# Kernel optimization log

Measured on AMD Instinct MI355X. Metric: run time of the kernel, lower is better.

The kernel has to match this reference:

```python
import jax, jax.numpy as jnp
import numpy as np

B, N, D, C = 256, 256, 512, 1024
EPS = 1e-12  # F.normalize eps


def _l2norm(x):
    n = jnp.linalg.norm(x, axis=-1, keepdims=True)
    return x / jnp.maximum(n, EPS)


def setup_inputs() -> dict:
    key = jax.random.key(0)
    k1, k2, k3 = jax.random.split(key, 3)
    return {
        "image_tokens": jax.random.normal(k1, (B, N, D), dtype=jnp.float32),
        "text_features": jax.random.normal(k2, (C, D), dtype=jnp.float32),
        "log_tau": jnp.asarray(np.log(0.07), dtype=jnp.float32),
        "log_attn_tau": jnp.asarray(np.log(0.07), dtype=jnp.float32),
        "pid_labels": jax.random.randint(k3, (B,), 0, C),
    }


def reference(image_tokens, text_features, log_tau, log_attn_tau, pid_labels):
    toks = _l2norm(image_tokens.astype(jnp.float32))        # [B,N,D]
    txt = _l2norm(text_features.astype(jnp.float32))        # [C,D]
    sims = jnp.einsum('bnd,cd->bnc', toks, txt)             # [B,N,C]
    gt = pid_labels.astype(jnp.int32)
    # sims[arange(B), :, gt] -> [B,N]
    sims_gt = jnp.take_along_axis(sims, gt[:, None, None], axis=2)[..., 0]
    attn_tau = jnp.clip(jnp.exp(log_attn_tau), 0.01, 1.0)
    w = jax.nn.softmax(sims_gt / attn_tau, axis=1)          # [B,N]
    logits = jnp.einsum('bn,bnc->bc', w, sims)              # [B,C]
    tau = jnp.clip(jnp.exp(log_tau), 0.01, 1.0)
    logits = logits / tau
    # cross_entropy with label_smoothing=0.0, mean reduction
    logp = jax.nn.log_softmax(logits, axis=-1)
    nll = -jnp.take_along_axis(logp, gt[:, None], axis=1)[:, 0]
    return jnp.mean(nll)
```

## Files before the change

kernel.cpp:

```cpp
#include <hip/hip_runtime.h>
#include <math.h>

#define Bb 256
#define Nn 256
#define Dd 512
#define Cc 1024
#define KC 8
#define KD (Dd / KC)

__device__ __forceinline__ float waveReduceSum(float v) {
    #pragma unroll
    for (int off = 32; off > 0; off >>= 1)
        v += __shfl_xor(v, off, 64);
    return v;
}
__device__ __forceinline__ float waveReduceMax(float v) {
    #pragma unroll
    for (int off = 32; off > 0; off >>= 1)
        v = fmaxf(v, __shfl_xor(v, off, 64));
    return v;
}

__global__ void k_txtnorm(const float* __restrict__ txt, float* __restrict__ txt_n) {
    const int c = blockIdx.x;
    const int lane = threadIdx.x;
    const float* row = txt + (size_t)c * Dd + lane * 8;
    float4 a = *(const float4*)row;
    float4 b = *(const float4*)(row + 4);
    float ss = a.x*a.x + a.y*a.y + a.z*a.z + a.w*a.w
             + b.x*b.x + b.y*b.y + b.z*b.z + b.w*b.w;
    ss = waveReduceSum(ss);
    const float inv = 1.0f / fmaxf(sqrtf(ss), 1e-12f);
    float* out = txt_n + (size_t)c * Dd + lane * 8;
    a.x *= inv; a.y *= inv; a.z *= inv; a.w *= inv;
    b.x *= inv; b.y *= inv; b.z *= inv; b.w *= inv;
    *(float4*)out = a;
    *(float4*)(out + 4) = b;
}

__global__ void k_transpose(const float* __restrict__ txt_n, float* __restrict__ txt_t) {
    __shared__ float tile[32][33];
    const int c0 = blockIdx.x * 32;
    const int d0 = blockIdx.y * 32;
    const int tx = threadIdx.x & 31;
    const int ty = threadIdx.x >> 5;
    #pragma unroll
    for (int r = ty; r < 32; r += 8)
        tile[r][tx] = txt_n[(size_t)(c0 + r) * Dd + d0 + tx];
    __syncthreads();
    #pragma unroll
    for (int r = ty; r < 32; r += 8)
        txt_t[(size_t)(d0 + r) * Cc + c0 + tx] = tile[tx][r];
}

__global__ void __launch_bounds__(1024) k_attn_q(const float* __restrict__ toks,
                                                 const float* __restrict__ txt_n,
                                                 const int* __restrict__ pid,
                                                 const float* __restrict__ log_attn_tau,
                                                 float* __restrict__ q) {
    const int b = blockIdx.x;
    const int tid = threadIdx.x;
    const int wv = tid >> 6;
    const int lane = tid & 63;
    __shared__ float xg[Dd];
    __shared__ float qpart_s[16][Dd];
    __shared__ float ms[16], Ss[16];
    const int g = pid[b];
    if (tid < Dd) xg[tid] = txt_n[(size_t)g * Dd + tid];
    __syncthreads();
    float at = expf(log_attn_tau[0]);
    at = fminf(fmaxf(at, 0.01f), 1.0f);
    const float iat = 1.0f / at;

    const float4 xg0 = *(const float4*)&xg[lane * 8];
    const float4 xg1 = *(const float4*)&xg[lane * 8 + 4];

    float m = -INFINITY, S = 0.0f;
    float qa[8] = {0.f, 0.f, 0.f, 0.f, 0.f, 0.f, 0.f, 0.f};

    const float* base = toks + ((size_t)b * Nn + wv * 16) * Dd + lane * 8;
    float4 t0 = *(const float4*)base;
    float4 t1 = *(const float4*)(base + 4);
    #pragma unroll 4
    for (int r = 0; r < 16; ++r) {
        float4 n0, n1;
        if (r < 15) {
            const float* p = base + (size_t)(r + 1) * Dd;
            n0 = *(const float4*)p;
            n1 = *(const float4*)(p + 4);
        }
        float dot = t0.x*xg0.x + t0.y*xg0.y + t0.z*xg0.z + t0.w*xg0.w
                  + t1.x*xg1.x + t1.y*xg1.y + t1.z*xg1.z + t1.w*xg1.w;
        float ss  = t0.x*t0.x + t0.y*t0.y + t0.z*t0.z + t0.w*t0.w
                  + t1.x*t1.x + t1.y*t1.y + t1.z*t1.z + t1.w*t1.w;
        dot = waveReduceSum(dot);
        ss = waveReduceSum(ss);
        const float inv = 1.0f / fmaxf(sqrtf(ss), 1e-12f);
        const float s = dot * inv;
        if (s > m) {
            const float sc = expf((m - s) * iat);
            S = S * sc + 1.0f;
            qa[0] = qa[0]*sc + inv*t0.x; qa[1] = qa[1]*sc + inv*t0.y;
            qa[2] = qa[2]*sc + inv*t0.z; qa[3] = qa[3]*sc + inv*t0.w;
            qa[4] = qa[4]*sc + inv*t1.x; qa[5] = qa[5]*sc + inv*t1.y;
            qa[6] = qa[6]*sc + inv*t1.z; qa[7] = qa[7]*sc + inv*t1.w;
            m = s;
        } else {
            const float e = expf((s - m) * iat);
            S += e;
            const float w = e * inv;
            qa[0] = fmaf(w, t0.x, qa[0]); qa[1] = fmaf(w, t0.y, qa[1]);
            qa[2] = fmaf(w, t0.z, qa[2]); qa[3] = fmaf(w, t0.w, qa[3]);
            qa[4] = fmaf(w, t1.x, qa[4]); qa[5] = fmaf(w, t1.y, qa[5]);
            qa[6] = fmaf(w, t1.z, qa[6]); qa[7] = fmaf(w, t1.w, qa[7]);
        }
        t0 = n0; t1 = n1;
    }
    #pragma unroll
    for (int j = 0; j < 8; ++j) qpart_s[wv][lane * 8 + j] = qa[j];
    if (lane == 0) { ms[wv] = m; Ss[wv] = S; }
    __syncthreads();
    if (tid < Dd) {
        float M = -INFINITY;
        #pragma unroll
        for (int w = 0; w < 16; ++w) M = fmaxf(M, ms[w]);
        float Stot = 0.f, acc = 0.f;
        #pragma unroll
        for (int w = 0; w < 16; ++w) {
            const float sc = expf((ms[w] - M) * iat);
            Stot = fmaf(Ss[w], sc, Stot);
            acc = fmaf(qpart_s[w][tid], sc, acc);
        }
        q[(size_t)b * Dd + tid] = acc / Stot;
    }
}

__global__ void k_logits(const float* __restrict__ q, const float* __restrict__ txt_t,
                         float* __restrict__ part) {
    const int b0 = blockIdx.x * 4;
    const int kc = blockIdx.y;
    const int d0 = kc * KD;
    const int t = threadIdx.x;
    __shared__ float qs[4][KD];
    {
        const int j = t >> 6, d = t & 63;
        qs[j][d] = q[(size_t)(b0 + j) * Dd + d0 + d];
    }
    __syncthreads();
    const float4* xt = (const float4*)txt_t;
    float4 a0 = {0,0,0,0}, a1 = {0,0,0,0}, a2 = {0,0,0,0}, a3 = {0,0,0,0};
    #pragma unroll 4
    for (int d = 0; d < KD; d += 4) {
        const float4 q0 = *(const float4*)&qs[0][d];
        const float4 q1 = *(const float4*)&qs[1][d];
        const float4 q2 = *(const float4*)&qs[2][d];
        const float4 q3 = *(const float4*)&qs[3][d];
        const float4 x0 = xt[(size_t)(d0 + d + 0) * (Cc / 4) + t];
        const float4 x1 = xt[(size_t)(d0 + d + 1) * (Cc / 4) + t];
        const float4 x2 = xt[(size_t)(d0 + d + 2) * (Cc / 4) + t];
        const float4 x3 = xt[(size_t)(d0 + d + 3) * (Cc / 4) + t];
        a0.x = fmaf(q0.x,x0.x,a0.x); a0.y = fmaf(q0.x,x0.y,a0.y); a0.z = fmaf(q0.x,x0.z,a0.z); a0.w = fmaf(q0.x,x0.w,a0.w);
        a0.x = fmaf(q0.y,x1.x,a0.x); a0.y = fmaf(q0.y,x1.y,a0.y); a0.z = fmaf(q0.y,x1.z,a0.z); a0.w = fmaf(q0.y,x1.w,a0.w);
        a0.x = fmaf(q0.z,x2.x,a0.x); a0.y = fmaf(q0.z,x2.y,a0.y); a0.z = fmaf(q0.z,x2.z,a0.z); a0.w = fmaf(q0.z,x2.w,a0.w);
        a0.x = fmaf(q0.w,x3.x,a0.x); a0.y = fmaf(q0.w,x3.y,a0.y); a0.z = fmaf(q0.w,x3.z,a0.z); a0.w = fmaf(q0.w,x3.w,a0.w);
        a1.x = fmaf(q1.x,x0.x,a1.x); a1.y = fmaf(q1.x,x0.y,a1.y); a1.z = fmaf(q1.x,x0.z,a1.z); a1.w = fmaf(q1.x,x0.w,a1.w);
        a1.x = fmaf(q1.y,x1.x,a1.x); a1.y = fmaf(q1.y,x1.y,a1.y); a1.z = fmaf(q1.y,x1.z,a1.z); a1.w = fmaf(q1.y,x1.w,a1.w);
        a1.x = fmaf(q1.z,x2.x,a1.x); a1.y = fmaf(q1.z,x2.y,a1.y); a1.z = fmaf(q1.z,x2.z,a1.z); a1.w = fmaf(q1.z,x2.w,a1.w);
        a1.x = fmaf(q1.w,x3.x,a1.x); a1.y = fmaf(q1.w,x3.y,a1.y); a1.z = fmaf(q1.w,x3.z,a1.z); a1.w = fmaf(q1.w,x3.w,a1.w);
        a2.x = fmaf(q2.x,x0.x,a2.x); a2.y = fmaf(q2.x,x0.y,a2.y); a2.z = fmaf(q2.x,x0.z,a2.z); a2.w = fmaf(q2.x,x0.w,a2.w);
        a2.x = fmaf(q2.y,x1.x,a2.x); a2.y = fmaf(q2.y,x1.y,a2.y); a2.z = fmaf(q2.y,x1.z,a2.z); a2.w = fmaf(q2.y,x1.w,a2.w);
        a2.x = fmaf(q2.z,x2.x,a2.x); a2.y = fmaf(q2.z,x2.y,a2.y); a2.z = fmaf(q2.z,x2.z,a2.z); a2.w = fmaf(q2.z,x2.w,a2.w);
        a2.x = fmaf(q2.w,x3.x,a2.x); a2.y = fmaf(q2.w,x3.y,a2.y); a2.z = fmaf(q2.w,x3.z,a2.z); a2.w = fmaf(q2.w,x3.w,a2.w);
        a3.x = fmaf(q3.x,x0.x,a3.x); a3.y = fmaf(q3.x,x0.y,a3.y); a3.z = fmaf(q3.x,x0.z,a3.z); a3.w = fmaf(q3.x,x0.w,a3.w);
        a3.x = fmaf(q3.y,x1.x,a3.x); a3.y = fmaf(q3.y,x1.y,a3.y); a3.z = fmaf(q3.y,x1.z,a3.z); a3.w = fmaf(q3.y,x1.w,a3.w);
        a3.x = fmaf(q3.z,x2.x,a3.x); a3.y = fmaf(q3.z,x2.y,a3.y); a3.z = fmaf(q3.z,x2.z,a3.z); a3.w = fmaf(q3.z,x2.w,a3.w);
        a3.x = fmaf(q3.w,x3.x,a3.x); a3.y = fmaf(q3.w,x3.y,a3.y); a3.z = fmaf(q3.w,x3.z,a3.z); a3.w = fmaf(q3.w,x3.w,a3.w);
    }
    float* pb = part + ((size_t)kc * Bb + b0) * Cc;
    ((float4*)(pb + 0 * Cc))[t] = a0;
    ((float4*)(pb + 1 * Cc))[t] = a1;
    ((float4*)(pb + 2 * Cc))[t] = a2;
    ((float4*)(pb + 3 * Cc))[t] = a3;
}

__global__ void k_lse(const float* __restrict__ part, const int* __restrict__ pid,
                      const float* __restrict__ log_tau, float* __restrict__ nll) {
    const int b = blockIdx.x;
    const int t = threadIdx.x;
    float4 l = {0,0,0,0};
    #pragma unroll
    for (int kc = 0; kc < KC; ++kc) {
        const float4 p = ((const float4*)(part + ((size_t)kc * Bb + b) * Cc))[t];
        l.x += p.x; l.y += p.y; l.z += p.z; l.w += p.w;
    }
    float tau = expf(log_tau[0]);
    tau = fminf(fmaxf(tau, 0.01f), 1.0f);
    const float itau = 1.0f / tau;
    l.x *= itau; l.y *= itau; l.z *= itau; l.w *= itau;

    const int g = pid[b];
    __shared__ float redm[4], reds[4], sgt;
    if ((g >> 2) == t) {
        const float v[4] = {l.x, l.y, l.z, l.w};
        sgt = v[g & 3];
    }
    float m = fmaxf(fmaxf(l.x, l.y), fmaxf(l.z, l.w));
    m = waveReduceMax(m);
    if ((t & 63) == 0) redm[t >> 6] = m;
    __syncthreads();
    m = fmaxf(fmaxf(redm[0], redm[1]), fmaxf(redm[2], redm[3]));
    float e = expf(l.x - m) + expf(l.y - m) + expf(l.z - m) + expf(l.w - m);
    e = waveReduceSum(e);
    if ((t & 63) == 0) reds[t >> 6] = e;
    __syncthreads();
    if (t == 0) {
        const float S = reds[0] + reds[1] + reds[2] + reds[3];
        nll[b] = m + logf(S) - sgt;
    }
}

__global__ void k_mean(const float* __restrict__ nll, float* __restrict__ out) {
    float v = nll[threadIdx.x];
    __shared__ float red[4];
    v = waveReduceSum(v);
    if ((threadIdx.x & 63) == 0) red[threadIdx.x >> 6] = v;
    __syncthreads();
    if (threadIdx.x == 0) out[0] = (red[0] + red[1] + red[2] + red[3]) * (1.0f / (float)Bb);
}

extern "C" void kernel_launch(void* const* d_in, const int* in_sizes, int n_in,
                              void* d_out, int out_size, void* d_ws, size_t ws_size,
                              hipStream_t stream) {
    const float* toks = (const float*)d_in[0];
    const float* txt = (const float*)d_in[1];
    const float* log_tau = (const float*)d_in[2];
    const float* log_attn_tau = (const float*)d_in[3];
    const int* pid = (const int*)d_in[4];
    float* out = (float*)d_out;

    float* ws = (float*)d_ws;
    float* txt_n = ws;
    float* txt_t = txt_n + (size_t)Cc * Dd;
    float* q     = txt_t + (size_t)Dd * Cc;
    float* part  = q + (size_t)Bb * Dd;
    float* nll   = part + (size_t)KC * Bb * Cc;

    k_txtnorm<<<Cc, 64, 0, stream>>>(txt, txt_n);
    k_transpose<<<dim3(Cc / 32, Dd / 32), 256, 0, stream>>>(txt_n, txt_t);
    k_attn_q<<<Bb, 1024, 0, stream>>>(toks, txt_n, pid, log_attn_tau, q);
    k_logits<<<dim3(Bb / 4, KC), 256, 0, stream>>>(q, txt_t, part);
    k_lse<<<Bb, 256, 0, stream>>>(part, pid, log_tau, nll);
    k_mean<<<1, 256, 0, stream>>>(nll, out);
}
```

Baseline: 218.8 us.

## Fuse text normalize with transpose, batch token loads, widen logits batch tile

Merges text normalization and transpose into one kernel that computes row norms and writes the normalized transposed matrix, which drops the intermediate normalized buffer and one launch. The attention kernel now normalizes the ground-truth text row itself. It also loads four token rows per batch and interleaves their shuffle reductions to expose more memory and instruction parallelism. The logits kernel processes 8 batch rows per block instead of 4 to reuse text loads more, at the cost of more registers and fewer blocks.

```diff
diff --git a/kernel.cpp b/kernel.cpp
--- a/kernel.cpp
+++ b/kernel.cpp
@@ -7,6 +7,7 @@
 #define Cc 1024
 #define KC 8
 #define KD (Dd / KC)
+#define BT 8
 
 __device__ __forceinline__ float waveReduceSum(float v) {
     #pragma unroll
@@ -21,40 +22,47 @@
     return v;
 }
 
-__global__ void k_txtnorm(const float* __restrict__ txt, float* __restrict__ txt_n) {
-    const int c = blockIdx.x;
-    const int lane = threadIdx.x;
-    const float* row = txt + (size_t)c * Dd + lane * 8;
-    float4 a = *(const float4*)row;
-    float4 b = *(const float4*)(row + 4);
-    float ss = a.x*a.x + a.y*a.y + a.z*a.z + a.w*a.w
-             + b.x*b.x + b.y*b.y + b.z*b.z + b.w*b.w;
-    ss = waveReduceSum(ss);
-    const float inv = 1.0f / fmaxf(sqrtf(ss), 1e-12f);
-    float* out = txt_n + (size_t)c * Dd + lane * 8;
-    a.x *= inv; a.y *= inv; a.z *= inv; a.w *= inv;
-    b.x *= inv; b.y *= inv; b.z *= inv; b.w *= inv;
-    *(float4*)out = a;
-    *(float4*)(out + 4) = b;
-}
-
-__global__ void k_transpose(const float* __restrict__ txt_n, float* __restrict__ txt_t) {
+__global__ void k_txt_prep(const float* __restrict__ txt, float* __restrict__ txt_t) {
+    __shared__ float ssp[32][8];
+    __shared__ float inv[32];
     __shared__ float tile[32][33];
     const int c0 = blockIdx.x * 32;
-    const int d0 = blockIdx.y * 32;
-    const int tx = threadIdx.x & 31;
-    const int ty = threadIdx.x >> 5;
-    #pragma unroll
-    for (int r = ty; r < 32; r += 8)
-        tile[r][tx] = txt_n[(size_t)(c0 + r) * Dd + d0 + tx];
-    __syncthreads();
-    #pragma unroll
-    for (int r = ty; r < 32; r += 8)
-        txt_t[(size_t)(d0 + r) * Cc + c0 + tx] = tile[tx][r];
+    const int t = threadIdx.x;
+    {
+        const int r = t >> 3, seg = t & 7;
+        const float4* p = (const float4*)(txt + (size_t)(c0 + r) * Dd + seg * 64);
+        float s = 0.f;
+        #pragma unroll
+        for (int i = 0; i < 16; ++i) {
+            const float4 a = p[i];
+            s += a.x*a.x + a.y*a.y + a.z*a.z + a.w*a.w;
+        }
+        ssp[r][seg] = s;
+    }
+    __syncthreads();
+    if (t < 32) {
+        float s = 0.f;
+        #pragma unroll
+        for (int j = 0; j < 8; ++j) s += ssp[t][j];
+        inv[t] = 1.0f / fmaxf(sqrtf(s), 1e-12f);
+    }
+    __syncthreads();
+    const int dx = t & 31, r4 = t >> 5;
+    const int dt0 = blockIdx.y * 128;
+    for (int dt = dt0; dt < dt0 + 128; dt += 32) {
+        #pragma unroll
+        for (int rr = r4; rr < 32; rr += 8)
+            tile[rr][dx] = txt[(size_t)(c0 + rr) * Dd + dt + dx] * inv[rr];
+        __syncthreads();
+        #pragma unroll
+        for (int rr = r4; rr < 32; rr += 8)
+            txt_t[(size_t)(dt + rr) * Cc + c0 + dx] = tile[dx][rr];
+        __syncthreads();
+    }
 }
 
 __global__ void __launch_bounds__(1024) k_attn_q(const float* __restrict__ toks,
-                                                 const float* __restrict__ txt_n,
+                                                 const float* __restrict__ txt,
                                                  const int* __restrict__ pid,
                                                  const float* __restrict__ log_attn_tau,
                                                  float* __restrict__ q) {
@@ -63,11 +71,22 @@
     const int wv = tid >> 6;
     const int lane = tid & 63;
     __shared__ float xg[Dd];
+    __shared__ float r8[8];
     __shared__ float qpart_s[16][Dd];
     __shared__ float ms[16], Ss[16];
+
     const int g = pid[b];
-    if (tid < Dd) xg[tid] = txt_n[(size_t)g * Dd + tid];
-    __syncthreads();
+    float v = 0.f;
+    if (tid < Dd) v = txt[(size_t)g * Dd + tid];
+    float p = v * v;
+    p = waveReduceSum(p);
+    if (lane == 0 && wv < 8) r8[wv] = p;
+    __syncthreads();
+    const float tot = r8[0]+r8[1]+r8[2]+r8[3]+r8[4]+r8[5]+r8[6]+r8[7];
+    const float invg = 1.0f / fmaxf(sqrtf(tot), 1e-12f);
+    if (tid < Dd) xg[tid] = v * invg;
+    __syncthreads();
+
     float at = expf(log_attn_tau[0]);
     at = fminf(fmaxf(at, 0.01f), 1.0f);
     const float iat = 1.0f / at;
@@ -78,43 +97,64 @@
     float m = -INFINITY, S = 0.0f;
     float qa[8] = {0.f, 0.f, 0.f, 0.f, 0.f, 0.f, 0.f, 0.f};
 
-    const float* base = toks + ((size_t)b * Nn + wv * 16) * Dd + lane * 8;
-    float4 t0 = *(const float4*)base;
-    float4 t1 = *(const float4*)(base + 4);
-    #pragma unroll 4
-    for (int r = 0; r < 16; ++r) {
-        float4 n0, n1;
-        if (r < 15) {
-            const float* p = base + (size_t)(r + 1) * Dd;
-            n0 = *(const float4*)p;
-            n1 = *(const float4*)(p + 4);
-        }
-        float dot = t0.x*xg0.x + t0.y*xg0.y + t0.z*xg0.z + t0.w*xg0.w
-                  + t1.x*xg1.x + t1.y*xg1.y + t1.z*xg1.z + t1.w*xg1.w;
-        float ss  = t0.x*t0.x + t0.y*t0.y + t0.z*t0.z + t0.w*t0.w
-                  + t1.x*t1.x + t1.y*t1.y + t1.z*t1.z + t1.w*t1.w;
-        dot = waveReduceSum(dot);
-        ss = waveReduceSum(ss);
-        const float inv = 1.0f / fmaxf(sqrtf(ss), 1e-12f);
-        const float s = dot * inv;
-        if (s > m) {
-            const float sc = expf((m - s) * iat);
-            S = S * sc + 1.0f;
-            qa[0] = qa[0]*sc + inv*t0.x; qa[1] = qa[1]*sc + inv*t0.y;
-            qa[2] = qa[2]*sc + inv*t0.z; qa[3] = qa[3]*sc + inv*t0.w;
-            qa[4] = qa[4]*sc + inv*t1.x; qa[5] = qa[5]*sc + inv*t1.y;
-            qa[6] = qa[6]*sc + inv*t1.z; qa[7] = qa[7]*sc + inv*t1.w;
-            m = s;
-        } else {
-            const float e = expf((s - m) * iat);
-            S += e;
-            const float w = e * inv;
-            qa[0] = fmaf(w, t0.x, qa[0]); qa[1] = fmaf(w, t0.y, qa[1]);
-            qa[2] = fmaf(w, t0.z, qa[2]); qa[3] = fmaf(w, t0.w, qa[3]);
-            qa[4] = fmaf(w, t1.x, qa[4]); qa[5] = fmaf(w, t1.y, qa[5]);
-            qa[6] = fmaf(w, t1.z, qa[6]); qa[7] = fmaf(w, t1.w, qa[7]);
-        }
-        t0 = n0; t1 = n1;
+    const float* base = toks + ((size_t)b * Nn + wv * 16) * Dd + (size_t)lane * 8;
+    float4 c0[4], c1[4];
+    #pragma unroll
+    for (int k = 0; k < 4; ++k) {
+        c0[k] = *(const float4*)(base + k * Dd);
+        c1[k] = *(const float4*)(base + k * Dd + 4);
+    }
+    #pragma unroll
+    for (int batch = 0; batch < 4; ++batch) {
+        float4 n0[4], n1[4];
+        if (batch < 3) {
+            const float* pn = base + (batch + 1) * 4 * Dd;
+            #pragma unroll
+            for (int k = 0; k < 4; ++k) {
+                n0[k] = *(const float4*)(pn + k * Dd);
+                n1[k] = *(const float4*)(pn + k * Dd + 4);
+            }
+        }
+        float dt[4], ss[4];
+        #pragma unroll
+        for (int k = 0; k < 4; ++k) {
+            dt[k] = c0[k].x*xg0.x + c0[k].y*xg0.y + c0[k].z*xg0.z + c0[k].w*xg0.w
+                  + c1[k].x*xg1.x + c1[k].y*xg1.y + c1[k].z*xg1.z + c1[k].w*xg1.w;
+            ss[k] = c0[k].x*c0[k].x + c0[k].y*c0[k].y + c0[k].z*c0[k].z + c0[k].w*c0[k].w
+                  + c1[k].x*c1[k].x + c1[k].y*c1[k].y + c1[k].z*c1[k].z + c1[k].w*c1[k].w;
+        }
+        #pragma unroll
+        for (int off = 32; off > 0; off >>= 1) {
+            #pragma unroll
+            for (int k = 0; k < 4; ++k) {
+                dt[k] += __shfl_xor(dt[k], off, 64);
+                ss[k] += __shfl_xor(ss[k], off, 64);
+            }
+        }
+        #pragma unroll
+        for (int k = 0; k < 4; ++k) {
+            const float inv = 1.0f / fmaxf(sqrtf(ss[k]), 1e-12f);
+            const float s = dt[k] * inv;
+            if (s > m) {
+                const float sc = expf((m - s) * iat);
+                S = S * sc + 1.0f;
+                qa[0] = qa[0]*sc + inv*c0[k].x; qa[1] = qa[1]*sc + inv*c0[k].y;
+                qa[2] = qa[2]*sc + inv*c0[k].z; qa[3] = qa[3]*sc + inv*c0[k].w;
+                qa[4] = qa[4]*sc + inv*c1[k].x; qa[5] = qa[5]*sc + inv*c1[k].y;
+                qa[6] = qa[6]*sc + inv*c1[k].z; qa[7] = qa[7]*sc + inv*c1[k].w;
+                m = s;
+            } else {
+                const float e = expf((s - m) * iat);
+                S += e;
+                const float w = e * inv;
+                qa[0] = fmaf(w, c0[k].x, qa[0]); qa[1] = fmaf(w, c0[k].y, qa[1]);
+                qa[2] = fmaf(w, c0[k].z, qa[2]); qa[3] = fmaf(w, c0[k].w, qa[3]);
+                qa[4] = fmaf(w, c1[k].x, qa[4]); qa[5] = fmaf(w, c1[k].y, qa[5]);
+                qa[6] = fmaf(w, c1[k].z, qa[6]); qa[7] = fmaf(w, c1[k].w, qa[7]);
+            }
+        }
+        #pragma unroll
+        for (int k = 0; k < 4; ++k) { c0[k] = n0[k]; c1[k] = n1[k]; }
     }
     #pragma unroll
     for (int j = 0; j < 8; ++j) qpart_s[wv][lane * 8 + j] = qa[j];
@@ -137,50 +177,36 @@
 
 __global__ void k_logits(const float* __restrict__ q, const float* __restrict__ txt_t,
                          float* __restrict__ part) {
-    const int b0 = blockIdx.x * 4;
+    const int b0 = blockIdx.x * BT;
     const int kc = blockIdx.y;
     const int d0 = kc * KD;
     const int t = threadIdx.x;
-    __shared__ float qs[4][KD];
-    {
-        const int j = t >> 6, d = t & 63;
-        qs[j][d] = q[(size_t)(b0 + j) * Dd + d0 + d];
-    }
+    __shared__ float qs[BT][KD];
+    for (int i = t; i < BT * KD; i += 256)
+        qs[i >> 6][i & 63] = q[(size_t)(b0 + (i >> 6)) * Dd + d0 + (i & 63)];
     __syncthreads();
     const float4* xt = (const float4*)txt_t;
-    float4 a0 = {0,0,0,0}, a1 = {0,0,0,0}, a2 = {0,0,0,0}, a3 = {0,0,0,0};
-    #pragma unroll 4
+    float4 a[BT];
+    #pragma unroll
+    for (int j = 0; j < BT; ++j) a[j] = make_float4(0.f, 0.f, 0.f, 0.f);
+    #pragma unroll 2
     for (int d = 0; d < KD; d += 4) {
-        const float4 q0 = *(const float4*)&qs[0][d];
-        const float4 q1 = *(const float4*)&qs[1][d];
-        const float4 q2 = *(const float4*)&qs[2][d];
-        const float4 q3 = *(const float4*)&qs[3][d];
         const float4 x0 = xt[(size_t)(d0 + d + 0) * (Cc / 4) + t];
         const float4 x1 = xt[(size_t)(d0 + d + 1) * (Cc / 4) + t];
         const float4 x2 = xt[(size_t)(d0 + d + 2) * (Cc / 4) + t];
         const float4 x3 = xt[(size_t)(d0 + d + 3) * (Cc / 4) + t];
-        a0.x = fmaf(q0.x,x0.x,a0.x); a0.y = fmaf(q0.x,x0.y,a0.y); a0.z = fmaf(q0.x,x0.z,a0.z); a0.w = fmaf(q0.x,x0.w,a0.w);
-        a0.x = fmaf(q0.y,x1.x,a0.x); a0.y = fmaf(q0.y,x1.y,a0.y); a0.z = fmaf(q0.y,x1.z,a0.z); a0.w = fmaf(q0.y,x1.w,a0.w);
-        a0.x = fmaf(q0.z,x2.x,a0.x); a0.y = fmaf(q0.z,x2.y,a0.y); a0.z = fmaf(q0.z,x2.z,a0.z); a0.w = fmaf(q0.z,x2.w,a0.w);
-        a0.x = fmaf(q0.w,x3.x,a0.x); a0.y = fmaf(q0.w,x3.y,a0.y); a0.z = fmaf(q0.w,x3.z,a0.z); a0.w = fmaf(q0.w,x3.w,a0.w);
-        a1.x = fmaf(q1.x,x0.x,a1.x); a1.y = fmaf(q1.x,x0.y,a1.y); a1.z = fmaf(q1.x,x0.z,a1.z); a1.w = fmaf(q1.x,x0.w,a1.w);
-        a1.x = fmaf(q1.y,x1.x,a1.x); a1.y = fmaf(q1.y,x1.y,a1.y); a1.z = fmaf(q1.y,x1.z,a1.z); a1.w = fmaf(q1.y,x1.w,a1.w);
-        a1.x = fmaf(q1.z,x2.x,a1.x); a1.y = fmaf(q1.z,x2.y,a1.y); a1.z = fmaf(q1.z,x2.z,a1.z); a1.w = fmaf(q1.z,x2.w,a1.w);
-        a1.x = fmaf(q1.w,x3.x,a1.x); a1.y = fmaf(q1.w,x3.y,a1.y); a1.z = fmaf(q1.w,x3.z,a1.z); a1.w = fmaf(q1.w,x3.w,a1.w);
-        a2.x = fmaf(q2.x,x0.x,a2.x); a2.y = fmaf(q2.x,x0.y,a2.y); a2.z = fmaf(q2.x,x0.z,a2.z); a2.w = fmaf(q2.x,x0.w,a2.w);
-        a2.x = fmaf(q2.y,x1.x,a2.x); a2.y = fmaf(q2.y,x1.y,a2.y); a2.z = fmaf(q2.y,x1.z,a2.z); a2.w = fmaf(q2.y,x1.w,a2.w);
-        a2.x = fmaf(q2.z,x2.x,a2.x); a2.y = fmaf(q2.z,x2.y,a2.y); a2.z = fmaf(q2.z,x2.z,a2.z); a2.w = fmaf(q2.z,x2.w,a2.w);
-        a2.x = fmaf(q2.w,x3.x,a2.x); a2.y = fmaf(q2.w,x3.y,a2.y); a2.z = fmaf(q2.w,x3.z,a2.z); a2.w = fmaf(q2.w,x3.w,a2.w);
-        a3.x = fmaf(q3.x,x0.x,a3.x); a3.y = fmaf(q3.x,x0.y,a3.y); a3.z = fmaf(q3.x,x0.z,a3.z); a3.w = fmaf(q3.x,x0.w,a3.w);
-        a3.x = fmaf(q3.y,x1.x,a3.x); a3.y = fmaf(q3.y,x1.y,a3.y); a3.z = fmaf(q3.y,x1.z,a3.z); a3.w = fmaf(q3.y,x1.w,a3.w);
-        a3.x = fmaf(q3.z,x2.x,a3.x); a3.y = fmaf(q3.z,x2.y,a3.y); a3.z = fmaf(q3.z,x2.z,a3.z); a3.w = fmaf(q3.z,x2.w,a3.w);
-        a3.x = fmaf(q3.w,x3.x,a3.x); a3.y = fmaf(q3.w,x3.y,a3.y); a3.z = fmaf(q3.w,x3.z,a3.z); a3.w = fmaf(q3.w,x3.w,a3.w);
+        #pragma unroll
+        for (int j = 0; j < BT; ++j) {
+            const float4 qj = *(const float4*)&qs[j][d];
+            a[j].x = fmaf(qj.x,x0.x,a[j].x); a[j].y = fmaf(qj.x,x0.y,a[j].y); a[j].z = fmaf(qj.x,x0.z,a[j].z); a[j].w = fmaf(qj.x,x0.w,a[j].w);
+            a[j].x = fmaf(qj.y,x1.x,a[j].x); a[j].y = fmaf(qj.y,x1.y,a[j].y); a[j].z = fmaf(qj.y,x1.z,a[j].z); a[j].w = fmaf(qj.y,x1.w,a[j].w);
+            a[j].x = fmaf(qj.z,x2.x,a[j].x); a[j].y = fmaf(qj.z,x2.y,a[j].y); a[j].z = fmaf(qj.z,x2.z,a[j].z); a[j].w = fmaf(qj.z,x2.w,a[j].w);
+            a[j].x = fmaf(qj.w,x3.x,a[j].x); a[j].y = fmaf(qj.w,x3.y,a[j].y); a[j].z = fmaf(qj.w,x3.z,a[j].z); a[j].w = fmaf(qj.w,x3.w,a[j].w);
+        }
     }
     float* pb = part + ((size_t)kc * Bb + b0) * Cc;
-    ((float4*)(pb + 0 * Cc))[t] = a0;
-    ((float4*)(pb + 1 * Cc))[t] = a1;
-    ((float4*)(pb + 2 * Cc))[t] = a2;
-    ((float4*)(pb + 3 * Cc))[t] = a3;
+    #pragma unroll
+    for (int j = 0; j < BT; ++j) ((float4*)(pb + (size_t)j * Cc))[t] = a[j];
 }
 
 __global__ void k_lse(const float* __restrict__ part, const int* __restrict__ pid,
@@ -239,16 +265,14 @@
     float* out = (float*)d_out;
 
     float* ws = (float*)d_ws;
-    float* txt_n = ws;
-    float* txt_t = txt_n + (size_t)Cc * Dd;
+    float* txt_t = ws;
     float* q     = txt_t + (size_t)Dd * Cc;
     float* part  = q + (size_t)Bb * Dd;
     float* nll   = part + (size_t)KC * Bb * Cc;
 
-    k_txtnorm<<<Cc, 64, 0, stream>>>(txt, txt_n);
-    k_transpose<<<dim3(Cc / 32, Dd / 32), 256, 0, stream>>>(txt_n, txt_t);
-    k_attn_q<<<Bb, 1024, 0, stream>>>(toks, txt_n, pid, log_attn_tau, q);
-    k_logits<<<dim3(Bb / 4, KC), 256, 0, stream>>>(q, txt_t, part);
+    k_txt_prep<<<dim3(Cc / 32, Dd / 128), 256, 0, stream>>>(txt, txt_t);
+    k_attn_q<<<Bb, 1024, 0, stream>>>(toks, txt, pid, log_attn_tau, q);
+    k_logits<<<dim3(Bb / BT, KC), 256, 0, stream>>>(q, txt_t, part);
     k_lse<<<Bb, 256, 0, stream>>>(part, pid, log_tau, nll);
     k_mean<<<1, 256, 0, stream>>>(nll, out);
 }
```

Result: no change. 219.6 us (+0.4%).
